# Kernel tuning notes

Measured on AMD Instinct MI355X. Metric: run time of the kernel, lower is better.

The kernel has to match this reference:

```python
import jax, jax.numpy as jnp
import numpy as np

B, C_IN, T, F = 8, 64, 128, 32
MAIN, AUX = 128, 64
D_IN, N_ST, DT_R = 256, 16, 8  # Mamba: d_inner=2*128, d_state=16, dt_rank=ceil(128/16)
SQ2 = 0.70710678
BN_S = 1.0 / np.sqrt(1.0 + 1e-5)  # eval BN with running stats (0,1)


def silu(x):
    return x * jax.nn.sigmoid(x)


def bn2d(x, g, b):
    return x * (g * BN_S)[None, :, None, None] + b[None, :, None, None]


def dwconv(x, w, b, pad):
    y = jax.lax.conv_general_dilated(
        x, w, (1, 1), ((pad, pad), (pad, pad)),
        dimension_numbers=('NCHW', 'OIHW', 'NCHW'),
        feature_group_count=x.shape[1])
    return y + b[None, :, None, None]


def mamba(x, in_w, conv_w, conv_b, xproj_w, dt_w, dt_b, A_log, D, out_w):
    # x: [B, L, d_model]
    Bsz, L, _ = x.shape
    xz = x @ in_w.T                       # [B,L,2*D_IN]
    xi, z = xz[..., :D_IN], xz[..., D_IN:]
    # causal depthwise conv1d, d_conv=4
    xp = jnp.pad(xi, ((0, 0), (3, 0), (0, 0)))
    xc = sum(xp[:, k:k + L, :] * conv_w[:, k] for k in range(4)) + conv_b
    xc = silu(xc)                          # [B,L,D_IN]
    x_dbl = xc @ xproj_w.T                 # [B,L,DT_R+2N]
    dt = jax.nn.softplus(x_dbl[..., :DT_R] @ dt_w.T + dt_b)   # [B,L,D_IN]
    Bt = x_dbl[..., DT_R:DT_R + N_ST]      # [B,L,N]
    Ct = x_dbl[..., DT_R + N_ST:]          # [B,L,N]
    A = -jnp.exp(A_log)                    # [D_IN,N]

    def step(h, inp):
        d_t, B_t, C_t, x_t = inp           # [B,D_IN],[B,N],[B,N],[B,D_IN]
        h = jnp.exp(d_t[..., None] * A) * h + (d_t * x_t)[..., None] * B_t[:, None, :]
        return h, jnp.einsum('bdn,bn->bd', h, C_t)

    h0 = jnp.zeros((Bsz, D_IN, N_ST), x.dtype)
    _, ys = jax.lax.scan(step, h0, (dt.transpose(1, 0, 2), Bt.transpose(1, 0, 2),
                                    Ct.transpose(1, 0, 2), xc.transpose(1, 0, 2)))
    y = ys.transpose(1, 0, 2) + D * xc
    return (y * silu(z)) @ out_w.T


def patch_proj(z, w, b, g, beta):
    bz, c, t2, f = z.shape
    zr = z.reshape(bz, c, t2, f // 2, 2)
    y = jnp.einsum('bctfp,ocp->botf', zr, w) + b[None, :, None, None]
    return jax.nn.relu(bn2d(y, g, beta))


def setup_inputs() -> dict:
    keys = iter(jax.random.split(jax.random.key(0), 64))

    def rn(shape, s=0.1):
        return jax.random.normal(next(keys), shape, jnp.float32) * s

    Alog = jnp.tile(jnp.log(jnp.arange(1, N_ST + 1, dtype=jnp.float32)), (D_IN, 1))
    d = {
        'x': rn((B, C_IN, T, F), 1.0),
        'main_w': rn((MAIN, C_IN, 2)), 'main_b': rn((MAIN,)),
        'main_g': jnp.ones((MAIN,)), 'main_beta': jnp.zeros((MAIN,)),
        'aux_w': rn((AUX, C_IN, 2)), 'aux_b': rn((AUX,)),
        'aux_g': jnp.ones((AUX,)), 'aux_beta': jnp.zeros((AUX,)),
        'ln_g': jnp.ones((MAIN,)), 'ln_b': jnp.zeros((MAIN,)),
        'vim_w': rn((MAIN, MAIN), 0.05), 'vim_b': jnp.zeros((MAIN,)),
        'mk3_w': rn((32, 1, 3, 3)), 'mk3_b': rn((32,)),
        'mk5_w': rn((32, 1, 5, 5)), 'mk5_b': rn((32,)),
        'mk_g': jnp.ones((AUX,)), 'mk_beta': jnp.zeros((AUX,)),
        'fus_w': rn((192, 192), 0.05), 'fus_b': jnp.zeros((192,)),
        'fus_g': jnp.ones((192,)), 'fus_beta': jnp.zeros((192,)),
        'rec_w': rn((192, C_IN, 2, 2), 0.05), 'rec_b': jnp.zeros((C_IN,)),
        'rec_g': jnp.ones((C_IN,)), 'rec_beta': jnp.zeros((C_IN,)),
    }
    for p in ('f', 'b'):
        d[p + '_in_w'] = rn((2 * D_IN, MAIN), 0.05)
        d[p + '_conv_w'] = rn((D_IN, 4))
        d[p + '_conv_b'] = rn((D_IN,))
        d[p + '_xproj_w'] = rn((DT_R + 2 * N_ST, D_IN), 0.05)
        d[p + '_dt_w'] = rn((D_IN, DT_R))
        d[p + '_dt_b'] = rn((D_IN,))
        d[p + '_Alog'] = Alog
        d[p + '_D'] = jnp.ones((D_IN,))
        d[p + '_out_w'] = rn((MAIN, D_IN), 0.05)
    return d


def reference(x, main_w, main_b, main_g, main_beta, aux_w, aux_b, aux_g, aux_beta,
              ln_g, ln_b,
              f_in_w, f_conv_w, f_conv_b, f_xproj_w, f_dt_w, f_dt_b, f_Alog, f_D, f_out_w,
              b_in_w, b_conv_w, b_conv_b, b_xproj_w, b_dt_w, b_dt_b, b_Alog, b_D, b_out_w,
              vim_w, vim_b, mk3_w, mk3_b, mk5_w, mk5_b, mk_g, mk_beta,
              fus_w, fus_b, fus_g, fus_beta, rec_w, rec_b, rec_g, rec_beta):
    # Haar wavelet along time (stride 2)
    xe, xo = x[:, :, 0::2, :], x[:, :, 1::2, :]
    low = (xe + xo) * SQ2
    high = (xo - xe) * SQ2                  # [B,C,T/2,F]
    main_in = patch_proj(low, main_w, main_b, main_g, main_beta)   # [B,128,T/2,F/2]
    aux_in = patch_proj(high, aux_w, aux_b, aux_g, aux_beta)       # [B,64,T/2,F/2]

    bz, c, h, w = main_in.shape
    x_seq = main_in.reshape(bz, c, h * w).transpose(0, 2, 1)       # [B,L,128]
    # VimBlock: LayerNorm -> bidirectional Mamba -> out_proj + residual
    mu = x_seq.mean(-1, keepdims=True)
    var = ((x_seq - mu) ** 2).mean(-1, keepdims=True)
    xn = (x_seq - mu) / jnp.sqrt(var + 1e-5) * ln_g + ln_b
    of = mamba(xn, f_in_w, f_conv_w, f_conv_b, f_xproj_w, f_dt_w, f_dt_b, f_Alog, f_D, f_out_w)
    ob = mamba(xn[:, ::-1, :], b_in_w, b_conv_w, b_conv_b, b_xproj_w, b_dt_w, b_dt_b,
               b_Alog, b_D, b_out_w)[:, ::-1, :]
    x_main_seq = (of + ob) @ vim_w.T + vim_b + x_seq
    x_main = x_main_seq.transpose(0, 2, 1).reshape(bz, c, h, w)

    # multi-kernel depthwise branch
    a1 = dwconv(aux_in[:, :32], mk3_w, mk3_b, 1)
    a2 = dwconv(aux_in[:, 32:], mk5_w, mk5_b, 2)
    x_aux = silu(bn2d(jnp.concatenate([a1, a2], axis=1), mk_g, mk_beta))

    x_in = jnp.concatenate([main_in, aux_in], axis=1)
    x_out = jnp.concatenate([x_main, x_aux], axis=1)
    fus = jnp.einsum('bcij,oc->boij', x_out, fus_w) + fus_b[None, :, None, None]
    x_fused = x_in + bn2d(fus, fus_g, fus_beta)

    # ConvTranspose2d kernel=stride=2 (non-overlapping) -> einsum + interleave reshape
    y = jnp.einsum('bcij,cokl->boikjl', x_fused, rec_w)
    y = y.reshape(bz, rec_w.shape[1], h * 2, w * 2) + rec_b[None, :, None, None]
    y = jax.nn.relu(bn2d(y, rec_g, rec_beta))
    return y + x
```

## Files before the change

### kernel.cpp

```cpp
#include <hip/hip_runtime.h>
#include <hip/hip_bf16.h>

#define SQ2F 0.70710678f
#define BNS 0.9999950000374997f
#define L_ 1024
#define TS 32
#define SEGL 128
#define WARM 64

typedef __attribute__((ext_vector_type(8))) short bf16x8;
typedef __attribute__((ext_vector_type(8))) unsigned short us8;
typedef __attribute__((ext_vector_type(4))) float f32x4;

__device__ __forceinline__ float silu_f(float v) { return v / (1.f + __expf(-v)); }
__device__ __forceinline__ unsigned short f2b(float f) {
    unsigned u = __float_as_uint(f);
    return (unsigned short)((u + 0x7FFFu + ((u >> 16) & 1u)) >> 16);
}

__global__ __launch_bounds__(256) void sentinel_sD(float* out, int n) {
    int i = blockIdx.x * 256 + threadIdx.x;
    if (i < n) out[i] = 1.0e6f;
}

__global__ __launch_bounds__(256) void wavelet_sD(const float* x, float* low, float* high, int b0) {
    int idx = blockIdx.x * 256 + threadIdx.x;
    int fq = idx & 31, i = (idx >> 5) & 63, c = (idx >> 11) & 63, bl = idx >> 17;
    size_t base = ((size_t)((b0 + bl) * 64 + c) * 128 + 2 * i) * 32 + fq;
    float xe = x[base];
    float xo = x[base + 32];
    int m = (bl * 64 + i) * 16 + (fq >> 1);
    int k = c * 2 + (fq & 1);
    low[(size_t)m * 128 + k]  = (xe + xo) * SQ2F;
    high[(size_t)m * 128 + k] = (xo - xe) * SQ2F;
}

__global__ __launch_bounds__(256) void wcvt_sD(
    const float* main_w, const float* aux_w, const float* in_w0, const float* in_w1,
    const float* xp0, const float* xp1, const float* vim_w, const float* fus_w,
    const float* ow0, const float* ow1, const float* rec_w, unsigned short* dst) {
    int i = blockIdx.x * 256 + threadIdx.x;
    float v;
    if      (i < 16384)  v = main_w[i];
    else if (i < 24576)  v = aux_w[i - 16384];
    else if (i < 90112)  v = in_w0[i - 24576];
    else if (i < 155648) v = in_w1[i - 90112];
    else if (i < 165888) v = xp0[i - 155648];
    else if (i < 176128) v = xp1[i - 165888];
    else if (i < 192512) v = vim_w[i - 176128];
    else if (i < 229376) v = fus_w[i - 192512];
    else if (i < 294912) {
        int j = i - 229376; int k = j & 511; int n = j >> 9;
        v = (k < 256) ? ow0[(size_t)n * 256 + k] : ow1[(size_t)n * 256 + (k - 256)];
    } else if (i < 344064) {
        int j = i - 294912; int n = j / 192, c = j % 192;
        v = rec_w[((size_t)(c * 64 + (n >> 2)) * 2 + ((n >> 1) & 1)) * 2 + (n & 1)];
    } else return;
    dst[i] = f2b(v);
}

__global__ __launch_bounds__(256) void mgemm_sD(
    const float* A, const float* A2, const unsigned short* W, float* C,
    int N, int K, int lda, int ldw, int ldc,
    int aflip, int cflip, int adual, int epi, int b0g, int agate,
    const float* bias, const float* gg, const float* bet,
    const float* xm, const float* xa, const float* xres, float* outf,
    const float* A1, const unsigned short* W1, float* C1, int N1, int aflip1,
    const float* bias1, const float* gg1, const float* bet1) {
    if (blockIdx.z) {
        A = A1; W = W1; C = C1; N = N1; aflip = aflip1;
        bias = bias1; gg = gg1; bet = bet1;
    }
    __shared__ unsigned short Ab[2][4][128][8];
    __shared__ unsigned short Wl[2][4][64][8];
    const int tid = threadIdx.x;
    const int wave = tid >> 6, lane = tid & 63;
    const int m0 = blockIdx.x * 128;
    const int n0 = blockIdx.y * 64;

    const int rA = tid >> 1, hA = tid & 1;
    const int nS = tid >> 2, gS = tid & 3;
    int m_a = m0 + rA;
    if (aflip) m_a ^= 1023;
    const float* Arow = A + (size_t)m_a * lda;
    const float* A2row = adual ? (A2 + (size_t)((m0 + rA) ^ 1023) * lda - 256) : Arow;
    const bool wok = (n0 + nS) < N;
    const unsigned short* Wrow = W + (size_t)(n0 + nS) * ldw;

    f32x4 acc[2][4];
#pragma unroll
    for (int i = 0; i < 2; ++i)
#pragma unroll
        for (int j = 0; j < 4; ++j) acc[i][j] = f32x4{0.f, 0.f, 0.f, 0.f};

    const int nk = K >> 5;
    float4 v0, v1, v2, v3;
    us8 wv;

    auto loadregs = [&](int kt) {
        const int k0 = kt * 32 + hA * 16;
        const float* src = (adual && k0 >= 256) ? A2row : Arow;
        v0 = *(const float4*)(src + k0);
        v1 = *(const float4*)(src + k0 + 4);
        v2 = *(const float4*)(src + k0 + 8);
        v3 = *(const float4*)(src + k0 + 12);
        if (agate) {
            float4 g0 = *(const float4*)(src + k0 + 256);
            float4 g1 = *(const float4*)(src + k0 + 260);
            float4 g2 = *(const float4*)(src + k0 + 264);
            float4 g3 = *(const float4*)(src + k0 + 268);
            v0.x *= silu_f(g0.x); v0.y *= silu_f(g0.y); v0.z *= silu_f(g0.z); v0.w *= silu_f(g0.w);
            v1.x *= silu_f(g1.x); v1.y *= silu_f(g1.y); v1.z *= silu_f(g1.z); v1.w *= silu_f(g1.w);
            v2.x *= silu_f(g2.x); v2.y *= silu_f(g2.y); v2.z *= silu_f(g2.z); v2.w *= silu_f(g2.w);
            v3.x *= silu_f(g3.x); v3.y *= silu_f(g3.y); v3.z *= silu_f(g3.z); v3.w *= silu_f(g3.w);
        }
        if (wok) wv = *(const us8*)(Wrow + kt * 32 + gS * 8);
        else     wv = us8{0, 0, 0, 0, 0, 0, 0, 0};
    };
    auto writelds = [&](int buf) {
        us8 lo, hi;
        lo[0] = f2b(v0.x); lo[1] = f2b(v0.y); lo[2] = f2b(v0.z); lo[3] = f2b(v0.w);
        lo[4] = f2b(v1.x); lo[5] = f2b(v1.y); lo[6] = f2b(v1.z); lo[7] = f2b(v1.w);
        hi[0] = f2b(v2.x); hi[1] = f2b(v2.y); hi[2] = f2b(v2.z); hi[3] = f2b(v2.w);
        hi[4] = f2b(v3.x); hi[5] = f2b(v3.y); hi[6] = f2b(v3.z); hi[7] = f2b(v3.w);
        *(us8*)&Ab[buf][2 * hA][rA][0] = lo;
        *(us8*)&Ab[buf][2 * hA + 1][rA][0] = hi;
        *(us8*)&Wl[buf][gS][nS][0] = wv;
    };

    loadregs(0);
    writelds(0);
    __syncthreads();

    const int li = lane & 15, kg = lane >> 4;
    for (int t = 0; t < nk; ++t) {
        if (t + 1 < nk) loadregs(t + 1);
        const int cb = t & 1;
        bf16x8 af0 = *(const bf16x8*)&Ab[cb][kg][wave * 32 + li][0];
        bf16x8 af1 = *(const bf16x8*)&Ab[cb][kg][wave * 32 + 16 + li][0];
        bf16x8 wf0 = *(const bf16x8*)&Wl[cb][kg][li][0];
        bf16x8 wf1 = *(const bf16x8*)&Wl[cb][kg][16 + li][0];
        bf16x8 wf2 = *(const bf16x8*)&Wl[cb][kg][32 + li][0];
        bf16x8 wf3 = *(const bf16x8*)&Wl[cb][kg][48 + li][0];
        acc[0][0] = __builtin_amdgcn_mfma_f32_16x16x32_bf16(af0, wf0, acc[0][0], 0, 0, 0);
        acc[0][1] = __builtin_amdgcn_mfma_f32_16x16x32_bf16(af0, wf1, acc[0][1], 0, 0, 0);
        acc[0][2] = __builtin_amdgcn_mfma_f32_16x16x32_bf16(af0, wf2, acc[0][2], 0, 0, 0);
        acc[0][3] = __builtin_amdgcn_mfma_f32_16x16x32_bf16(af0, wf3, acc[0][3], 0, 0, 0);
        acc[1][0] = __builtin_amdgcn_mfma_f32_16x16x32_bf16(af1, wf0, acc[1][0], 0, 0, 0);
        acc[1][1] = __builtin_amdgcn_mfma_f32_16x16x32_bf16(af1, wf1, acc[1][1], 0, 0, 0);
        acc[1][2] = __builtin_amdgcn_mfma_f32_16x16x32_bf16(af1, wf2, acc[1][2], 0, 0, 0);
        acc[1][3] = __builtin_amdgcn_mfma_f32_16x16x32_bf16(af1, wf3, acc[1][3], 0, 0, 0);
        if (t + 1 < nk) writelds((t + 1) & 1);
        __syncthreads();
    }

#pragma unroll
    for (int mf = 0; mf < 2; ++mf) {
#pragma unroll
        for (int nf = 0; nf < 4; ++nf) {
#pragma unroll
            for (int rr = 0; rr < 4; ++rr) {
                int m = m0 + wave * 32 + mf * 16 + (lane >> 4) * 4 + rr;
                int n = n0 + nf * 16 + (lane & 15);
                if (n >= N) continue;
                float v = acc[mf][nf][rr];
                int bb = m >> 10, l = m & 1023;
                if (epi == 0) {
                    int mm = cflip ? (m ^ 1023) : m;
                    C[(size_t)mm * ldc + n] = v;
                } else if (epi == 1) {
                    v += bias[n];
                    v = v * (gg[n] * BNS) + bet[n];
                    C[((size_t)(bb * N + n) << 10) + l] = fmaxf(v, 0.f);
                } else if (epi == 2) {
                    C[(size_t)m * ldc + n] = v + bias[n] + xm[((size_t)(bb * 128 + n) << 10) + l];
                } else if (epi == 3) {
                    float xin = (n < 128) ? xm[((size_t)(bb * 128 + n) << 10) + l]
                                          : xa[((size_t)(bb * 64 + (n - 128)) << 10) + l];
                    C[(size_t)m * ldc + n] = xin + (v + bias[n]) * (gg[n] * BNS) + bet[n];
                } else {
                    int o = n >> 2, kq = (n >> 1) & 1, l2 = n & 1;
                    int ii = l >> 4, jj = l & 15;
                    v += bias[o];
                    v = fmaxf(v * (gg[o] * BNS) + bet[o], 0.f);
                    size_t oidx = ((size_t)((b0g + bb) * 64 + o) * 128 + (2 * ii + kq)) * 32 + (2 * jj + l2);
                    outf[oidx] = v + xres[oidx];
                }
            }
        }
    }
}

__global__ __launch_bounds__(256) void ln_sD(const float* mainin, const float* g,
                                             const float* bt, float* xn) {
    __shared__ float tile[128][65];
    __shared__ float red0[4][64];
    __shared__ float red1[4][64];
    __shared__ float mu_s[64];
    __shared__ float rs_s[64];
    const int bb = blockIdx.y;
    const int l0 = blockIdx.x * 64;
    const int tid = threadIdx.x;
    for (int idx = tid; idx < 128 * 64; idx += 256) {
        int c = idx >> 6, l = idx & 63;
        tile[c][l] = mainin[((size_t)(bb * 128 + c) << 10) + l0 + l];
    }
    __syncthreads();
    {
        int l = tid & 63, q = tid >> 6;
        float s = 0.f, s2 = 0.f;
#pragma unroll
        for (int c0 = 0; c0 < 32; ++c0) {
            float v = tile[q * 32 + c0][l];
            s += v; s2 = fmaf(v, v, s2);
        }
        red0[q][l] = s; red1[q][l] = s2;
    }
    __syncthreads();
    if (tid < 64) {
        float S = red0[0][tid] + red0[1][tid] + red0[2][tid] + red0[3][tid];
        float S2 = red1[0][tid] + red1[1][tid] + red1[2][tid] + red1[3][tid];
        float mu = S * (1.f / 128.f);
        float var = S2 * (1.f / 128.f) - mu * mu;
        mu_s[tid] = mu;
        rs_s[tid] = rsqrtf(var + 1e-5f);
    }
    __syncthreads();
    for (int idx = tid; idx < 128 * 64; idx += 256) {
        int l = idx >> 7, c = idx & 127;
        float v = (tile[c][l] - mu_s[l]) * rs_s[l] * g[c] + bt[c];
        xn[((size_t)(bb << 10) + l0 + l) * 128 + c] = v;
    }
}

__global__ __launch_bounds__(256) void conv_sD(const float* xzf, const float* xzb,
                                               const float* cw0, const float* cb0,
                                               const float* cw1, const float* cb1,
                                               float* xcf, float* xcb2) {
    int m = blockIdx.x, d = threadIdx.x, dir = blockIdx.y;
    const float* xz = dir ? xzb : xzf;
    const float* cw = dir ? cw1 : cw0;
    const float* cb = dir ? cb1 : cb0;
    float* xc = dir ? xcb2 : xcf;
    int l = m & 1023;
    float acc = cb[d];
    const float* w = cw + d * 4;
    for (int k = 0; k < 4; ++k) {
        int ls = l - 3 + k;
        if (ls >= 0) acc = fmaf(xz[(size_t)(m - 3 + k) * 512 + d], w[k], acc);
    }
    xc[(size_t)m * 256 + d] = silu_f(acc);
}

#define STAGE_SD(L0V, SBV)                                                                  \
    {                                                                                       \
        const int l0_ = (L0V), sb_ = (SBV);                                                 \
        _Pragma("unroll")                                                                   \
        for (int f = t2; f < TS * 4; f += 64) {                                             \
            int l = f >> 2, sg = (f & 3) * 4;                                               \
            *(float4*)&xvs[sb_][l][sg] = *(const float4*)(xcb + base256 + (size_t)(l0_ + l) * 256 + sg); \
        }                                                                                   \
        _Pragma("unroll")                                                                   \
        for (int f = t2; f < TS * 10; f += 64) {                                            \
            int l = f / 10, p = f % 10;                                                     \
            float4 v = *(const float4*)(xdb + base40 + (size_t)(l0_ + l) * 40 + p * 4);     \
            if (p < 2) *(float4*)&xd8[sb_][l][p * 4] = v;                                   \
            else       *(float4*)&bcs[sb_][l][p * 4 - 8] = v;                               \
        }                                                                                   \
        {                                                                                   \
            int dd = t2 & 15, lb = (t2 >> 4) * 8;                                           \
            float4 wA = *(const float4*)&dtw_s[dd][0];                                      \
            float4 wB = *(const float4*)&dtw_s[dd][4];                                      \
            float bsv = dtb_s[dd];                                                          \
            _Pragma("unroll")                                                               \
            for (int vv = 0; vv < 8; ++vv) {                                                \
                int l = lb + vv;                                                            \
                float4 xA = *(const float4*)&xd8[sb_][l][0];                                \
                float4 xB = *(const float4*)&xd8[sb_][l][4];                                \
                float a_ = bsv;                                                             \
                a_ = fmaf(xA.x, wA.x, a_); a_ = fmaf(xA.y, wA.y, a_);                       \
                a_ = fmaf(xA.z, wA.z, a_); a_ = fmaf(xA.w, wA.w, a_);                       \
                a_ = fmaf(xB.x, wB.x, a_); a_ = fmaf(xB.y, wB.y, a_);                       \
                a_ = fmaf(xB.z, wB.z, a_); a_ = fmaf(xB.w, wB.w, a_);                       \
                dts[sb_][l][dd] = (a_ > 15.f) ? a_ : log1pf(__expf(a_));                    \
            }                                                                               \
        }                                                                                   \
    }

__global__ __launch_bounds__(128) void scan_sD(
    const float* xc0, const float* xc1, const float* xd0, const float* xd1,
    const float* dtw0, const float* dtw1, const float* dtbv0, const float* dtbv1,
    const float* al0, const float* al1, const float* D0, const float* D1,
    float* y0, float* y1) {
    __shared__ float dts[2][TS][16];
    __shared__ float xvs[2][TS][16];
    __shared__ float bcs[2][TS][32];
    __shared__ float xd8[2][TS][8];
    __shared__ float dtw_s[16][8];
    __shared__ float dtb_s[16];

    const int b = blockIdx.x;
    const int dir = blockIdx.y;
    const int seg = blockIdx.z >> 4;
    const int d0 = (blockIdx.z & 15) * 16;
    const int tid = threadIdx.x;

    const float* xcb = dir ? xc1 : xc0;
    const float* xdb = dir ? xd1 : xd0;
    float* ygb = dir ? y1 : y0;

    const size_t base256 = (size_t)b * L_ * 256 + d0;
    const size_t base40  = (size_t)b * L_ * 40;

    const int lstart = seg * SEGL - (seg ? WARM : 0);
    const int ntiles = (seg ? (SEGL + WARM) : SEGL) / TS;
    const int wtiles = seg ? (WARM / TS) : 0;

    const int isStage = tid >> 6;
    const int t2 = tid & 63;
    const int dg = t2 >> 2, q = t2 & 3;

    const float LOG2E = 1.44269504088896340736f;
    float al2[4];
    float Dd = 0.f;
    float h0 = 0.f, h1 = 0.f, h2 = 0.f, h3 = 0.f;
    if (!isStage) {
        const float* alog = (dir ? al1 : al0) + (d0 + dg) * 16 + q * 4;
#pragma unroll
        for (int n = 0; n < 4; ++n) al2[n] = -__expf(alog[n]) * LOG2E;
        Dd = (dir ? D1 : D0)[d0 + dg];
    } else {
        const float* dtw = dir ? dtw1 : dtw0;
        const float* dtbv = dir ? dtbv1 : dtbv0;
        for (int i = t2; i < 128; i += 64)
            dtw_s[i >> 3][i & 7] = dtw[(size_t)(d0 + (i >> 3)) * 8 + (i & 7)];
        if (t2 < 16) dtb_s[t2] = dtbv[d0 + t2];
    }
    float* yp = ygb + (size_t)b * L_ * 512 + d0 + dg;

    if (isStage) STAGE_SD(lstart, 0);
    __syncthreads();

    for (int t = 0; t < ntiles; ++t) {
        if (isStage) {
            if (t + 1 < ntiles) STAGE_SD(lstart + (t + 1) * TS, (t + 1) & 1);
        } else {
            const int cb = t & 1;
            const bool dostore = (t >= wtiles);
#pragma unroll 4
            for (int l = 0; l < TS; ++l) {
                float dt = dts[cb][l][dg];
                float xv = xvs[cb][l][dg];
                float4 Bv = *(const float4*)&bcs[cb][l][q * 4];
                float4 Cv = *(const float4*)&bcs[cb][l][16 + q * 4];
                float dtx = dt * xv;
                float e0 = exp2f(dt * al2[0]);
                float e1 = exp2f(dt * al2[1]);
                float e2 = exp2f(dt * al2[2]);
                float e3 = exp2f(dt * al2[3]);
                h0 = fmaf(e0, h0, dtx * Bv.x);
                h1 = fmaf(e1, h1, dtx * Bv.y);
                h2 = fmaf(e2, h2, dtx * Bv.z);
                h3 = fmaf(e3, h3, dtx * Bv.w);
                float acc = fmaf(h3, Cv.w, fmaf(h2, Cv.z, fmaf(h1, Cv.y, h0 * Cv.x)));
                acc += __shfl_xor(acc, 1);
                acc += __shfl_xor(acc, 2);
                if (dostore && q == 0) {
                    yp[(size_t)(lstart + t * TS + l) * 512] = fmaf(Dd, xv, acc);
                }
            }
        }
        __syncthreads();
    }
}

__global__ __launch_bounds__(256) void dwconv_sD(const float* auxin,
                                                 const float* mk3w, const float* mk3b,
                                                 const float* mk5w, const float* mk5b,
                                                 const float* mkg, const float* mkbeta,
                                                 float* xout) {
    int idx = blockIdx.x * 256 + threadIdx.x;
    int j = idx & 15, i = (idx >> 4) & 63, c = (idx >> 10) & 63, b = idx >> 16;
    const float* src = auxin + ((size_t)(b * 64 + c) << 10);
    float acc;
    if (c < 32) {
        acc = mk3b[c];
        for (int di = -1; di <= 1; ++di)
            for (int dj = -1; dj <= 1; ++dj) {
                int ii = i + di, jj = j + dj;
                if (ii >= 0 && ii < 64 && jj >= 0 && jj < 16)
                    acc = fmaf(src[ii * 16 + jj], mk3w[(c * 3 + di + 1) * 3 + dj + 1], acc);
            }
    } else {
        int cc = c - 32;
        acc = mk5b[cc];
        for (int di = -2; di <= 2; ++di)
            for (int dj = -2; dj <= 2; ++dj) {
                int ii = i + di, jj = j + dj;
                if (ii >= 0 && ii < 64 && jj >= 0 && jj < 16)
                    acc = fmaf(src[ii * 16 + jj], mk5w[(cc * 5 + di + 2) * 5 + dj + 2], acc);
            }
    }
    float v = acc * (mkg[c] * BNS) + mkbeta[c];
    v = silu_f(v);
    xout[(size_t)((b << 10) + i * 16 + j) * 192 + 128 + c] = v;
}

extern "C" void kernel_launch(void* const* d_in, const int* in_sizes, int n_in,
                              void* d_out, int out_size, void* d_ws, size_t ws_size,
                              hipStream_t stream) {
    (void)in_sizes; (void)n_in;
    const float* X         = (const float*)d_in[0];
    const float* main_w    = (const float*)d_in[1];
    const float* main_b    = (const float*)d_in[2];
    const float* main_g    = (const float*)d_in[3];
    const float* main_beta = (const float*)d_in[4];
    const float* aux_w     = (const float*)d_in[5];
    const float* aux_b     = (const float*)d_in[6];
    const float* aux_g     = (const float*)d_in[7];
    const float* aux_beta  = (const float*)d_in[8];
    const float* ln_g      = (const float*)d_in[9];
    const float* ln_b      = (const float*)d_in[10];
    const float* vim_w     = (const float*)d_in[11];
    const float* vim_b     = (const float*)d_in[12];
    const float* mk3_w     = (const float*)d_in[13];
    const float* mk3_b     = (const float*)d_in[14];
    const float* mk5_w     = (const float*)d_in[15];
    const float* mk5_b     = (const float*)d_in[16];
    const float* mk_g      = (const float*)d_in[17];
    const float* mk_beta   = (const float*)d_in[18];
    const float* fus_w     = (const float*)d_in[19];
    const float* fus_b     = (const float*)d_in[20];
    const float* fus_g     = (const float*)d_in[21];
    const float* fus_beta  = (const float*)d_in[22];
    const float* rec_w     = (const float*)d_in[23];
    const float* rec_b     = (const float*)d_in[24];
    const float* rec_g     = (const float*)d_in[25];
    const float* rec_beta  = (const float*)d_in[26];
    const float* in_w0    = (const float*)d_in[27];
    const float* conv_w0  = (const float*)d_in[28];
    const float* conv_b0  = (const float*)d_in[29];
    const float* xproj_w0 = (const float*)d_in[30];
    const float* dt_w0    = (const float*)d_in[31];
    const float* dt_b0    = (const float*)d_in[32];
    const float* Alog0    = (const float*)d_in[33];
    const float* Dvec0    = (const float*)d_in[34];
    const float* out_w0   = (const float*)d_in[35];
    const float* in_w1    = (const float*)d_in[36];
    const float* conv_w1  = (const float*)d_in[37];
    const float* conv_b1  = (const float*)d_in[38];
    const float* xproj_w1 = (const float*)d_in[39];
    const float* dt_w1    = (const float*)d_in[40];
    const float* dt_b1    = (const float*)d_in[41];
    const float* Alog1    = (const float*)d_in[42];
    const float* Dvec1    = (const float*)d_in[43];
    const float* out_w1   = (const float*)d_in[44];

    const size_t wf = ws_size / sizeof(float);
    const size_t FIX = 172032;
    int nb = 0;
    if      (FIX + (size_t)8 * 1024 * 2576 <= wf) nb = 8;
    else if (FIX + (size_t)4 * 1024 * 2576 <= wf) nb = 4;
    else if (FIX + (size_t)2 * 1024 * 2576 <= wf) nb = 2;
    else if (FIX + (size_t)1 * 1024 * 2576 <= wf) nb = 1;
    if (nb == 0) {
        sentinel_sD<<<(out_size + 255) / 256, 256, 0, stream>>>((float*)d_out, out_size);
        return;
    }

    float* ws = (float*)d_ws;
    unsigned short* warena = (unsigned short*)ws;
    const unsigned short* bmain = warena;
    const unsigned short* baux  = warena + 16384;
    const unsigned short* bin0  = warena + 24576;
    const unsigned short* bin1  = warena + 90112;
    const unsigned short* bxp0  = warena + 155648;
    const unsigned short* bxp1  = warena + 165888;
    const unsigned short* bvim  = warena + 176128;
    const unsigned short* bfus  = warena + 192512;
    const unsigned short* bwcat = warena + 229376;
    const unsigned short* brec  = warena + 294912;

    const size_t R = (size_t)nb * 1024;
    float* xzf    = ws + FIX;
    float* xzb    = xzf + R * 512;
    float* mainin = xzb + R * 512;
    float* auxin  = mainin + R * 128;
    float* xn     = auxin + R * 64;
    float* vimin  = xn;
    float* lowb   = xn + R * 128;
    float* highb  = lowb + R * 128;
    float* xcf    = highb + R * 128;
    float* xcb    = xcf + R * 256;
    float* xoutc  = xcf;
    float* xfused = xcb;
    float* xdblf  = xcb + R * 256;
    float* xdblb  = xdblf + R * 40;

    wcvt_sD<<<1344, 256, 0, stream>>>(main_w, aux_w, in_w0, in_w1, xproj_w0, xproj_w1,
                                      vim_w, fus_w, out_w0, out_w1, rec_w, warena);
    const unsigned GM = (unsigned)(R / 128);

    for (int b0 = 0; b0 < 8; b0 += nb) {
        wavelet_sD<<<nb * 512, 256, 0, stream>>>(X, lowb, highb, b0);

        mgemm_sD<<<dim3(GM, 2, 2), 256, 0, stream>>>(
            lowb, nullptr, bmain, mainin, 128, 128, 128, 128, 0, 0, 0, 0, 1, 0, 0,
            main_b, main_g, main_beta, nullptr, nullptr, nullptr, nullptr,
            highb, baux, auxin, 64, 0, aux_b, aux_g, aux_beta);
        ln_sD<<<dim3(16, nb), 256, 0, stream>>>(mainin, ln_g, ln_b, xn);

        mgemm_sD<<<dim3(GM, 8, 2), 256, 0, stream>>>(
            xn, nullptr, bin0, xzf, 512, 128, 128, 128, 512, 0, 0, 0, 0, 0, 0,
            nullptr, nullptr, nullptr, nullptr, nullptr, nullptr, nullptr,
            xn, bin1, xzb, 512, 1, nullptr, nullptr, nullptr);

        conv_sD<<<dim3((unsigned)R, 2), 256, 0, stream>>>(
            xzf, xzb, conv_w0, conv_b0, conv_w1, conv_b1, xcf, xcb);

        mgemm_sD<<<dim3(GM, 1, 2), 256, 0, stream>>>(
            xcf, nullptr, bxp0, xdblf, 40, 256, 256, 256, 40, 0, 0, 0, 0, 0, 0,
            nullptr, nullptr, nullptr, nullptr, nullptr, nullptr, nullptr,
            xcb, bxp1, xdblb, 40, 0, nullptr, nullptr, nullptr);

        scan_sD<<<dim3(nb, 2, 128), 128, 0, stream>>>(
            xcf, xcb, xdblf, xdblb, dt_w0, dt_w1, dt_b0, dt_b1,
            Alog0, Alog1, Dvec0, Dvec1, xzf, xzb);

        mgemm_sD<<<dim3(GM, 2, 1), 256, 0, stream>>>(
            xzf, xzb, bwcat, vimin, 128, 512, 512, 512, 128, 0, 0, 1, 0, 0, 1,
            nullptr, nullptr, nullptr, nullptr, nullptr, nullptr, nullptr,
            nullptr, nullptr, nullptr, 0, 0, nullptr, nullptr, nullptr);

        mgemm_sD<<<dim3(GM, 2, 1), 256, 0, stream>>>(
            vimin, nullptr, bvim, xoutc, 128, 128, 128, 128, 192, 0, 0, 0, 2, 0, 0,
            vim_b, nullptr, nullptr, mainin, nullptr, nullptr, nullptr,
            nullptr, nullptr, nullptr, 0, 0, nullptr, nullptr, nullptr);

        dwconv_sD<<<nb * 256, 256, 0, stream>>>(
            auxin, mk3_w, mk3_b, mk5_w, mk5_b, mk_g, mk_beta, xoutc);

        mgemm_sD<<<dim3(GM, 3, 1), 256, 0, stream>>>(
            xoutc, nullptr, bfus, xfused, 192, 192, 192, 192, 192, 0, 0, 0, 3, 0, 0,
            fus_b, fus_g, fus_beta, mainin, auxin, nullptr, nullptr,
            nullptr, nullptr, nullptr, 0, 0, nullptr, nullptr, nullptr);

        mgemm_sD<<<dim3(GM, 4, 1), 256, 0, stream>>>(
            xfused, nullptr, brec, nullptr, 256, 192, 192, 192, 0, 0, 0, 0, 4, b0, 0,
            rec_b, rec_g, rec_beta, nullptr, nullptr, X, (float*)d_out,
            nullptr, nullptr, nullptr, 0, 0, nullptr, nullptr, nullptr);
    }
}
```

Baseline: 247.3 us.

## Fold dt projection into x_proj weights and compute softplus dt in GEMM

Precomputes a composite weight, dt_w @ xproj_w[:8], in bf16 and appends it to the x_proj weight so the x_proj GEMM directly produces the 256-wide dt with bias and softplus in a new epilogue, alongside B and C. The scan kernel no longer computes the rank-8 dt projection per tile; it just loads precomputed dt. This moves work from the latency-bound scan to the MFMA GEMM but adds a 256-wide fp32 dt write and read per direction, and changes rounding because the composed weight is stored in bf16.

New measurement: 241.6 us. 1.02x faster.

```diff
diff --git a/kernel.cpp b/kernel.cpp
--- a/kernel.cpp
+++ b/kernel.cpp
@@ -18,12 +18,16 @@
     return (unsigned short)((u + 0x7FFFu + ((u >> 16) & 1u)) >> 16);
 }
 
-__global__ __launch_bounds__(256) void sentinel_sD(float* out, int n) {
+#define AR_XPC0 155648
+#define AR_XPC1 229376
+#define AR_END  471040
+
+__global__ __launch_bounds__(256) void sentinel_sE(float* out, int n) {
     int i = blockIdx.x * 256 + threadIdx.x;
     if (i < n) out[i] = 1.0e6f;
 }
 
-__global__ __launch_bounds__(256) void wavelet_sD(const float* x, float* low, float* high, int b0) {
+__global__ __launch_bounds__(256) void wavelet_sE(const float* x, float* low, float* high, int b0) {
     int idx = blockIdx.x * 256 + threadIdx.x;
     int fq = idx & 31, i = (idx >> 5) & 63, c = (idx >> 11) & 63, bl = idx >> 17;
     size_t base = ((size_t)((b0 + bl) * 64 + c) * 128 + 2 * i) * 32 + fq;
@@ -35,7 +39,7 @@
     high[(size_t)m * 128 + k] = (xo - xe) * SQ2F;
 }
 
-__global__ __launch_bounds__(256) void wcvt_sD(
+__global__ __launch_bounds__(256) void wcvt_sE(
     const float* main_w, const float* aux_w, const float* in_w0, const float* in_w1,
     const float* xp0, const float* xp1, const float* vim_w, const float* fus_w,
     const float* ow0, const float* ow1, const float* rec_w, unsigned short* dst) {
@@ -45,31 +49,47 @@
     else if (i < 24576)  v = aux_w[i - 16384];
     else if (i < 90112)  v = in_w0[i - 24576];
     else if (i < 155648) v = in_w1[i - 90112];
-    else if (i < 165888) v = xp0[i - 155648];
-    else if (i < 176128) v = xp1[i - 165888];
-    else if (i < 192512) v = vim_w[i - 176128];
-    else if (i < 229376) v = fus_w[i - 192512];
-    else if (i < 294912) {
-        int j = i - 229376; int k = j & 511; int n = j >> 9;
+    else if (i < 163840) { int j = i - 155648; v = xp0[(size_t)((j >> 8) + 8) * 256 + (j & 255)]; }
+    else if (i < 229376) return;
+    else if (i < 237568) { int j = i - 229376; v = xp1[(size_t)((j >> 8) + 8) * 256 + (j & 255)]; }
+    else if (i < 303104) return;
+    else if (i < 319488) v = vim_w[i - 303104];
+    else if (i < 356352) v = fus_w[i - 319488];
+    else if (i < 421888) {
+        int j = i - 356352; int k = j & 511; int n = j >> 9;
         v = (k < 256) ? ow0[(size_t)n * 256 + k] : ow1[(size_t)n * 256 + (k - 256)];
-    } else if (i < 344064) {
-        int j = i - 294912; int n = j / 192, c = j % 192;
+    } else if (i < AR_END) {
+        int j = i - 421888; int n = j / 192, c = j % 192;
         v = rec_w[((size_t)(c * 64 + (n >> 2)) * 2 + ((n >> 1) & 1)) * 2 + (n & 1)];
     } else return;
     dst[i] = f2b(v);
 }
 
-__global__ __launch_bounds__(256) void mgemm_sD(
+__global__ __launch_bounds__(256) void wcomp_sE(const float* xp0, const float* xp1,
+                                                const float* dtw0, const float* dtw1,
+                                                unsigned short* arena) {
+    int idx = blockIdx.x * 256 + threadIdx.x;
+    int dir = blockIdx.y;
+    int d = idx >> 8, k = idx & 255;
+    const float* xp = dir ? xp1 : xp0;
+    const float* dtw = dir ? dtw1 : dtw0;
+    float v = 0.f;
+#pragma unroll
+    for (int r = 0; r < 8; ++r) v = fmaf(dtw[d * 8 + r], xp[(size_t)r * 256 + k], v);
+    arena[(size_t)(dir ? AR_XPC1 : AR_XPC0) + (size_t)(32 + d) * 256 + k] = f2b(v);
+}
+
+__global__ __launch_bounds__(256) void mgemm_sE(
     const float* A, const float* A2, const unsigned short* W, float* C,
     int N, int K, int lda, int ldw, int ldc,
     int aflip, int cflip, int adual, int epi, int b0g, int agate,
     const float* bias, const float* gg, const float* bet,
     const float* xm, const float* xa, const float* xres, float* outf,
     const float* A1, const unsigned short* W1, float* C1, int N1, int aflip1,
-    const float* bias1, const float* gg1, const float* bet1) {
+    const float* bias1, const float* gg1, const float* bet1, float* outf1) {
     if (blockIdx.z) {
         A = A1; W = W1; C = C1; N = N1; aflip = aflip1;
-        bias = bias1; gg = gg1; bet = bet1;
+        bias = bias1; gg = gg1; bet = bet1; outf = outf1;
     }
     __shared__ unsigned short Ab[2][4][128][8];
     __shared__ unsigned short Wl[2][4][64][8];
@@ -178,20 +198,28 @@
                     float xin = (n < 128) ? xm[((size_t)(bb * 128 + n) << 10) + l]
                                           : xa[((size_t)(bb * 64 + (n - 128)) << 10) + l];
                     C[(size_t)m * ldc + n] = xin + (v + bias[n]) * (gg[n] * BNS) + bet[n];
-                } else {
+                } else if (epi == 4) {
                     int o = n >> 2, kq = (n >> 1) & 1, l2 = n & 1;
                     int ii = l >> 4, jj = l & 15;
                     v += bias[o];
                     v = fmaxf(v * (gg[o] * BNS) + bet[o], 0.f);
                     size_t oidx = ((size_t)((b0g + bb) * 64 + o) * 128 + (2 * ii + kq)) * 32 + (2 * jj + l2);
                     outf[oidx] = v + xres[oidx];
+                } else {
+                    if (n < 32) {
+                        C[(size_t)m * 32 + n] = v;
+                    } else {
+                        float a = v + bias[n - 32];
+                        float sp = (a > 15.f) ? a : __logf(1.f + __expf(a));
+                        outf[(size_t)m * 256 + (n - 32)] = sp;
+                    }
                 }
             }
         }
     }
 }
 
-__global__ __launch_bounds__(256) void ln_sD(const float* mainin, const float* g,
+__global__ __launch_bounds__(256) void ln_sE(const float* mainin, const float* g,
                                              const float* bt, float* xn) {
     __shared__ float tile[128][65];
     __shared__ float red0[4][64];
@@ -233,7 +261,7 @@
     }
 }
 
-__global__ __launch_bounds__(256) void conv_sD(const float* xzf, const float* xzb,
+__global__ __launch_bounds__(256) void conv_sE(const float* xzf, const float* xzb,
                                                const float* cw0, const float* cb0,
                                                const float* cw1, const float* cb1,
                                                float* xcf, float* xcb2) {
@@ -252,52 +280,30 @@
     xc[(size_t)m * 256 + d] = silu_f(acc);
 }
 
-#define STAGE_SD(L0V, SBV)                                                                  \
+#define STAGE_SE(L0V, SBV)                                                                  \
     {                                                                                       \
         const int l0_ = (L0V), sb_ = (SBV);                                                 \
         _Pragma("unroll")                                                                   \
         for (int f = t2; f < TS * 4; f += 64) {                                             \
             int l = f >> 2, sg = (f & 3) * 4;                                               \
             *(float4*)&xvs[sb_][l][sg] = *(const float4*)(xcb + base256 + (size_t)(l0_ + l) * 256 + sg); \
+            *(float4*)&dts[sb_][l][sg] = *(const float4*)(dlb + base256 + (size_t)(l0_ + l) * 256 + sg); \
         }                                                                                   \
         _Pragma("unroll")                                                                   \
-        for (int f = t2; f < TS * 10; f += 64) {                                            \
-            int l = f / 10, p = f % 10;                                                     \
-            float4 v = *(const float4*)(xdb + base40 + (size_t)(l0_ + l) * 40 + p * 4);     \
-            if (p < 2) *(float4*)&xd8[sb_][l][p * 4] = v;                                   \
-            else       *(float4*)&bcs[sb_][l][p * 4 - 8] = v;                               \
+        for (int f = t2; f < TS * 8; f += 64) {                                             \
+            int l = f >> 3, sg = (f & 7) * 4;                                               \
+            *(float4*)&bcs[sb_][l][sg] = *(const float4*)(xdb + base32 + (size_t)(l0_ + l) * 32 + sg);   \
         }                                                                                   \
-        {                                                                                   \
-            int dd = t2 & 15, lb = (t2 >> 4) * 8;                                           \
-            float4 wA = *(const float4*)&dtw_s[dd][0];                                      \
-            float4 wB = *(const float4*)&dtw_s[dd][4];                                      \
-            float bsv = dtb_s[dd];                                                          \
-            _Pragma("unroll")                                                               \
-            for (int vv = 0; vv < 8; ++vv) {                                                \
-                int l = lb + vv;                                                            \
-                float4 xA = *(const float4*)&xd8[sb_][l][0];                                \
-                float4 xB = *(const float4*)&xd8[sb_][l][4];                                \
-                float a_ = bsv;                                                             \
-                a_ = fmaf(xA.x, wA.x, a_); a_ = fmaf(xA.y, wA.y, a_);                       \
-                a_ = fmaf(xA.z, wA.z, a_); a_ = fmaf(xA.w, wA.w, a_);                       \
-                a_ = fmaf(xB.x, wB.x, a_); a_ = fmaf(xB.y, wB.y, a_);                       \
-                a_ = fmaf(xB.z, wB.z, a_); a_ = fmaf(xB.w, wB.w, a_);                       \
-                dts[sb_][l][dd] = (a_ > 15.f) ? a_ : log1pf(__expf(a_));                    \
-            }                                                                               \
-        }                                                                                   \
-    }
-
-__global__ __launch_bounds__(128) void scan_sD(
-    const float* xc0, const float* xc1, const float* xd0, const float* xd1,
-    const float* dtw0, const float* dtw1, const float* dtbv0, const float* dtbv1,
+    }
+
+__global__ __launch_bounds__(128) void scan_sE(
+    const float* xc0, const float* xc1, const float* dtl0, const float* dtl1,
+    const float* xd0, const float* xd1,
     const float* al0, const float* al1, const float* D0, const float* D1,
     float* y0, float* y1) {
     __shared__ float dts[2][TS][16];
     __shared__ float xvs[2][TS][16];
     __shared__ float bcs[2][TS][32];
-    __shared__ float xd8[2][TS][8];
-    __shared__ float dtw_s[16][8];
-    __shared__ float dtb_s[16];
 
     const int b = blockIdx.x;
     const int dir = blockIdx.y;
@@ -306,11 +312,12 @@
     const int tid = threadIdx.x;
 
     const float* xcb = dir ? xc1 : xc0;
+    const float* dlb = dir ? dtl1 : dtl0;
     const float* xdb = dir ? xd1 : xd0;
     float* ygb = dir ? y1 : y0;
 
     const size_t base256 = (size_t)b * L_ * 256 + d0;
-    const size_t base40  = (size_t)b * L_ * 40;
+    const size_t base32  = (size_t)b * L_ * 32;
 
     const int lstart = seg * SEGL - (seg ? WARM : 0);
     const int ntiles = (seg ? (SEGL + WARM) : SEGL) / TS;
@@ -329,21 +336,15 @@
 #pragma unroll
         for (int n = 0; n < 4; ++n) al2[n] = -__expf(alog[n]) * LOG2E;
         Dd = (dir ? D1 : D0)[d0 + dg];
-    } else {
-        const float* dtw = dir ? dtw1 : dtw0;
-        const float* dtbv = dir ? dtbv1 : dtbv0;
-        for (int i = t2; i < 128; i += 64)
-            dtw_s[i >> 3][i & 7] = dtw[(size_t)(d0 + (i >> 3)) * 8 + (i & 7)];
-        if (t2 < 16) dtb_s[t2] = dtbv[d0 + t2];
     }
     float* yp = ygb + (size_t)b * L_ * 512 + d0 + dg;
 
-    if (isStage) STAGE_SD(lstart, 0);
+    if (isStage) STAGE_SE(lstart, 0);
     __syncthreads();
 
     for (int t = 0; t < ntiles; ++t) {
         if (isStage) {
-            if (t + 1 < ntiles) STAGE_SD(lstart + (t + 1) * TS, (t + 1) & 1);
+            if (t + 1 < ntiles) STAGE_SE(lstart + (t + 1) * TS, (t + 1) & 1);
         } else {
             const int cb = t & 1;
             const bool dostore = (t >= wtiles);
@@ -374,7 +375,7 @@
     }
 }
 
-__global__ __launch_bounds__(256) void dwconv_sD(const float* auxin,
+__global__ __launch_bounds__(256) void dwconv_sE(const float* auxin,
                                                  const float* mk3w, const float* mk3b,
                                                  const float* mk5w, const float* mk5b,
                                                  const float* mkg, const float* mkbeta,
@@ -457,14 +458,14 @@
     const float* out_w1   = (const float*)d_in[44];
 
     const size_t wf = ws_size / sizeof(float);
-    const size_t FIX = 172032;
+    const size_t FIX = AR_END / 2;
     int nb = 0;
-    if      (FIX + (size_t)8 * 1024 * 2576 <= wf) nb = 8;
-    else if (FIX + (size_t)4 * 1024 * 2576 <= wf) nb = 4;
-    else if (FIX + (size_t)2 * 1024 * 2576 <= wf) nb = 2;
-    else if (FIX + (size_t)1 * 1024 * 2576 <= wf) nb = 1;
+    if      (FIX + (size_t)8 * 1024 * 2432 <= wf) nb = 8;
+    else if (FIX + (size_t)4 * 1024 * 2432 <= wf) nb = 4;
+    else if (FIX + (size_t)2 * 1024 * 2432 <= wf) nb = 2;
+    else if (FIX + (size_t)1 * 1024 * 2432 <= wf) nb = 1;
     if (nb == 0) {
-        sentinel_sD<<<(out_size + 255) / 256, 256, 0, stream>>>((float*)d_out, out_size);
+        sentinel_sE<<<(out_size + 255) / 256, 256, 0, stream>>>((float*)d_out, out_size);
         return;
     }
 
@@ -474,12 +475,12 @@
     const unsigned short* baux  = warena + 16384;
     const unsigned short* bin0  = warena + 24576;
     const unsigned short* bin1  = warena + 90112;
-    const unsigned short* bxp0  = warena + 155648;
-    const unsigned short* bxp1  = warena + 165888;
-    const unsigned short* bvim  = warena + 176128;
-    const unsigned short* bfus  = warena + 192512;
-    const unsigned short* bwcat = warena + 229376;
-    const unsigned short* brec  = warena + 294912;
+    const unsigned short* bxpc0 = warena + AR_XPC0;
+    const unsigned short* bxpc1 = warena + AR_XPC1;
+    const unsigned short* bvim  = warena + 303104;
+    const unsigned short* bfus  = warena + 319488;
+    const unsigned short* bwcat = warena + 356352;
+    const unsigned short* brec  = warena + 421888;
 
     const size_t R = (size_t)nb * 1024;
     float* xzf    = ws + FIX;
@@ -490,64 +491,67 @@
     float* vimin  = xn;
     float* lowb   = xn + R * 128;
     float* highb  = lowb + R * 128;
+    float* dtlf   = lowb;
     float* xcf    = highb + R * 128;
     float* xcb    = xcf + R * 256;
     float* xoutc  = xcf;
     float* xfused = xcb;
     float* xdblf  = xcb + R * 256;
-    float* xdblb  = xdblf + R * 40;
-
-    wcvt_sD<<<1344, 256, 0, stream>>>(main_w, aux_w, in_w0, in_w1, xproj_w0, xproj_w1,
+    float* xdblb  = xdblf + R * 32;
+    float* dtlb   = xdblb + R * 32;
+
+    wcvt_sE<<<1840, 256, 0, stream>>>(main_w, aux_w, in_w0, in_w1, xproj_w0, xproj_w1,
                                       vim_w, fus_w, out_w0, out_w1, rec_w, warena);
+    wcomp_sE<<<dim3(256, 2), 256, 0, stream>>>(xproj_w0, xproj_w1, dt_w0, dt_w1, warena);
     const unsigned GM = (unsigned)(R / 128);
 
     for (int b0 = 0; b0 < 8; b0 += nb) {
-        wavelet_sD<<<nb * 512, 256, 0, stream>>>(X, lowb, highb, b0);
-
-        mgemm_sD<<<dim3(GM, 2, 2), 256, 0, stream>>>(
+        wavelet_sE<<<nb * 512, 256, 0, stream>>>(X, lowb, highb, b0);
+
+        mgemm_sE<<<dim3(GM, 2, 2), 256, 0, stream>>>(
             lowb, nullptr, bmain, mainin, 128, 128, 128, 128, 0, 0, 0, 0, 1, 0, 0,
             main_b, main_g, main_beta, nullptr, nullptr, nullptr, nullptr,
-            highb, baux, auxin, 64, 0, aux_b, aux_g, aux_beta);
-        ln_sD<<<dim3(16, nb), 256, 0, stream>>>(mainin, ln_g, ln_b, xn);
-
-        mgemm_sD<<<dim3(GM, 8, 2), 256, 0, stream>>>(
+            highb, baux, auxin, 64, 0, aux_b, aux_g, aux_beta, nullptr);
+        ln_sE<<<dim3(16, nb), 256, 0, stream>>>(mainin, ln_g, ln_b, xn);
+
+        mgemm_sE<<<dim3(GM, 8, 2), 256, 0, stream>>>(
             xn, nullptr, bin0, xzf, 512, 128, 128, 128, 512, 0, 0, 0, 0, 0, 0,
             nullptr, nullptr, nullptr, nullptr, nullptr, nullptr, nullptr,
-            xn, bin1, xzb, 512, 1, nullptr, nullptr, nullptr);
-
-        conv_sD<<<dim3((unsigned)R, 2), 256, 0, stream>>>(
+            xn, bin1, xzb, 512, 1, nullptr, nullptr, nullptr, nullptr);
+
+        conv_sE<<<dim3((unsigned)R, 2), 256, 0, stream>>>(
             xzf, xzb, conv_w0, conv_b0, conv_w1, conv_b1, xcf, xcb);
 
-        mgemm_sD<<<dim3(GM, 1, 2), 256, 0, stream>>>(
-            xcf, nullptr, bxp0, xdblf, 40, 256, 256, 256, 40, 0, 0, 0, 0, 0, 0,
-            nullptr, nullptr, nullptr, nullptr, nullptr, nullptr, nullptr,
-            xcb, bxp1, xdblb, 40, 0, nullptr, nullptr, nullptr);
-
-        scan_sD<<<dim3(nb, 2, 128), 128, 0, stream>>>(
-            xcf, xcb, xdblf, xdblb, dt_w0, dt_w1, dt_b0, dt_b1,
+        mgemm_sE<<<dim3(GM, 5, 2), 256, 0, stream>>>(
+            xcf, nullptr, bxpc0, xdblf, 288, 256, 256, 256, 32, 0, 0, 0, 5, 0, 0,
+            dt_b0, nullptr, nullptr, nullptr, nullptr, nullptr, dtlf,
+            xcb, bxpc1, xdblb, 288, 0, dt_b1, nullptr, nullptr, dtlb);
+
+        scan_sE<<<dim3(nb, 2, 128), 128, 0, stream>>>(
+            xcf, xcb, dtlf, dtlb, xdblf, xdblb,
             Alog0, Alog1, Dvec0, Dvec1, xzf, xzb);
 
-        mgemm_sD<<<dim3(GM, 2, 1), 256, 0, stream>>>(
+        mgemm_sE<<<dim3(GM, 2, 1), 256, 0, stream>>>(
             xzf, xzb, bwcat, vimin, 128, 512, 512, 512, 128, 0, 0, 1, 0, 0, 1,
             nullptr, nullptr, nullptr, nullptr, nullptr, nullptr, nullptr,
-            nullptr, nullptr, nullptr, 0, 0, nullptr, nullptr, nullptr);
-
-        mgemm_sD<<<dim3(GM, 2, 1), 256, 0, stream>>>(
+            nullptr, nullptr, nullptr, 0, 0, nullptr, nullptr, nullptr, nullptr);
+
+        mgemm_sE<<<dim3(GM, 2, 1), 256, 0, stream>>>(
             vimin, nullptr, bvim, xoutc, 128, 128, 128, 128, 192, 0, 0, 0, 2, 0, 0,
             vim_b, nullptr, nullptr, mainin, nullptr, nullptr, nullptr,
-            nullptr, nullptr, nullptr, 0, 0, nullptr, nullptr, nullptr);
-
-        dwconv_sD<<<nb * 256, 256, 0, stream>>>(
+            nullptr, nullptr, nullptr, 0, 0, nullptr, nullptr, nullptr, nullptr);
+
+        dwconv_sE<<<nb * 256, 256, 0, stream>>>(
             auxin, mk3_w, mk3_b, mk5_w, mk5_b, mk_g, mk_beta, xoutc);
 
-        mgemm_sD<<<dim3(GM, 3, 1), 256, 0, stream>>>(
+        mgemm_sE<<<dim3(GM, 3, 1), 256, 0, stream>>>(
             xoutc, nullptr, bfus, xfused, 192, 192, 192, 192, 192, 0, 0, 0, 3, 0, 0,
             fus_b, fus_g, fus_beta, mainin, auxin, nullptr, nullptr,
-            nullptr, nullptr, nullptr, 0, 0, nullptr, nullptr, nullptr);
-
-        mgemm_sD<<<dim3(GM, 4, 1), 256, 0, stream>>>(
+            nullptr, nullptr, nullptr, 0, 0, nullptr, nullptr, nullptr, nullptr);
+
+        mgemm_sE<<<dim3(GM, 4, 1), 256, 0, stream>>>(
             xfused, nullptr, brec, nullptr, 256, 192, 192, 192, 0, 0, 0, 0, 4, b0, 0,
             rec_b, rec_g, rec_beta, nullptr, nullptr, X, (float*)d_out,
-            nullptr, nullptr, nullptr, 0, 0, nullptr, nullptr, nullptr);
-    }
-}
+            nullptr, nullptr, nullptr, 0, 0, nullptr, nullptr, nullptr, nullptr);
+    }
+}
```
